# Kernel tuning notes

Measured on AMD Instinct MI355X. Metric: run time of the kernel, lower is better.

The kernel has to match this reference:

```python
import jax, jax.numpy as jnp
import numpy as np
jax.config.update("jax_enable_x64", True)

WINDOW_SHAPE = (16, 16, 8)
SPARSE_SHAPE = (512, 512, 64)
GROUP_SIZE = 128
BATCH_COUNTS = np.array([500000, 480123, 510007, 495870], dtype=np.int64)  # not multiples of 128 -> padding path active


def setup_inputs() -> dict:
    key = jax.random.key(0)
    kx, ky, kz = jax.random.split(key, 3)
    N = int(BATCH_COUNTS.sum())
    bids = jnp.asarray(np.repeat(np.arange(len(BATCH_COUNTS), dtype=np.int64), BATCH_COUNTS))
    x = jax.random.randint(kx, (N,), 0, SPARSE_SHAPE[0], dtype=jnp.int64)
    y = jax.random.randint(ky, (N,), 0, SPARSE_SHAPE[1], dtype=jnp.int64)
    z = jax.random.randint(kz, (N,), 0, SPARSE_SHAPE[2], dtype=jnp.int64)
    coords = jnp.stack([bids, x, y, z], axis=1)  # [N,4] int64: (batch, x, y, z)
    return {"coords": coords, "batch_size": 4}


def _hash_keys(coords, shifted):
    n, m, l = SPARSE_SHAPE
    n2o, m2o, l2o = WINDOW_SHAPE
    n1 = int(np.ceil(n / n2o) + 1)
    m1 = int(np.ceil(m / m2o) + 1)
    l1 = int(np.ceil(l / l2o) + 1)
    if shifted:
        x = coords[:, 1] + n2o // 2
        y = coords[:, 2] + m2o // 2
        z = coords[:, 3] + l2o // 2
    else:
        x, y, z = coords[:, 1], coords[:, 2], coords[:, 3]
    x1, y1, z1 = x // n2o, y // m2o, z // l2o
    x2, y2, z2 = x % n2o, y % m2o, z % l2o
    # original code triples both window and grid-of-window extents before hashing
    n2, m2, l2 = 3 * n2o, 3 * m2o, 3 * l2o
    n1, m1, l1 = 3 * n1, 3 * m1, 3 * l1
    sx = 1 - 2 * (x1 & 1)  # (-1)**x1
    sy = 1 - 2 * (y1 & 1)
    sz = 1 - 2 * (z1 & 1)
    s2x = 1 - 2 * (x2 & 1)
    s2y = 1 - 2 * (y2 & 1)
    s2z = 1 - 2 * (z2 & 1)
    boff = coords[:, 0] * (n * m * l * 10)
    vx = (n1 * y1 + n1 * m1 * z1 + sy * x1) * (n2 * m2 * l2) + sy * (m2 * x2 + n2 * m2 * z2 + s2x * y2) + boff
    vy = (m1 * z1 + m1 * l1 * x1 + sz * y1) * (m2 * l2 * n2) + sz * (l2 * y2 + m2 * l2 * x2 + s2y * z2) + boff
    vz = (l1 * x1 + l1 * n1 * y1 + sx * z1) * (l2 * n2 * m2) + sx * (n2 * z2 + l2 * n2 * y2 + s2z * x2) + boff
    return vx, vy, vz


def reference(coords, batch_size):
    G = GROUP_SIZE
    coords = coords.astype(jnp.int64)
    bids = coords[:, 0]
    N = coords.shape[0]
    num_per_batch = jax.ops.segment_sum(jnp.ones((N,), jnp.int64), bids, num_segments=batch_size)
    bs = jnp.concatenate([jnp.zeros((1,), jnp.int64), jnp.cumsum(num_per_batch)])
    num_per_batch_p = ((num_per_batch + G - 1) // G) * G
    bsp = jnp.concatenate([jnp.zeros((1,), jnp.int64), jnp.cumsum(num_per_batch_p)])
    Np = int(bsp[-1])  # concrete (not under jit); padded total length

    # win2flat[j] = j + (bsp[b] - bs[b]) for b = batch of element j (coords assumed batch-sorted)
    win2flat = jnp.arange(N, dtype=jnp.int64) + (bsp[:-1] - bs[:-1])[bids]

    # flat2win: identity within each padded batch, with the padded tail replicated
    # from one group earlier, then shifted back to flat indexing.
    p = jnp.arange(Np, dtype=jnp.int64)
    b = jnp.searchsorted(bsp, p, side="right") - 1  # batch of each padded slot
    r = num_per_batch % G
    pad_tail = (r[b] != 0) & (p >= bsp[b + 1] - G + r[b])
    flat2win = p - G * pad_tail.astype(jnp.int64) - (bsp[b] - bs[b])

    outs = [flat2win, win2flat]
    for shifted in (False, True):
        vx, vy, vz = _hash_keys(coords, shifted)
        outs.append(jnp.argsort(vx))
        outs.append(jnp.argsort(vy))
        outs.append(jnp.argsort(vz))
    # (flat2win, win2flat, x, y, z, x_shift, y_shift, z_shift)
    return tuple(outs)
```

## Files before the change

### kernel.cpp

```cpp
#include <hip/hip_runtime.h>
#include <type_traits>

typedef unsigned long long u64;
typedef unsigned int u32;

#define BLOCK     256
#define WAVES     4
#define TILE      4096
#define SUBT      1024
#define CHUNKS    16
#define KSHIFT    21
#define KBIAS     (1LL << 21)
#define KMASK     ((1u << 21) - 1)
#define GRP       128


__device__ __forceinline__ void hash3(long long x, long long y, long long z,
                                      long long boff, long long* v) {
  long long x1 = x >> 4, y1 = y >> 4, z1 = z >> 3;
  long long x2 = x & 15, y2 = y & 15, z2 = z & 7;
  long long sx  = 1 - 2*(x1 & 1), sy  = 1 - 2*(y1 & 1), sz  = 1 - 2*(z1 & 1);
  long long s2x = 1 - 2*(x2 & 1), s2y = 1 - 2*(y2 & 1), s2z = 1 - 2*(z2 & 1);
  v[0] = (99*y1 + 9801*z1 + sy*x1)*55296 + sy*(48*x2 + 2304*z2 + s2x*y2) + boff;
  v[1] = (99*z1 + 2673*x1 + sz*y1)*55296 + sz*(24*y2 + 1152*x2 + s2y*z2) + boff;
  v[2] = (27*x1 + 2673*y1 + sx*z1)*55296 + sx*(48*z2 + 1152*y2 + s2z*x2) + boff;
}

__global__ void count_k(const int* __restrict__ coords, unsigned* __restrict__ counts, int N) {
  __shared__ unsigned c[8];
  if (threadIdx.x < 8) c[threadIdx.x] = 0;
  __syncthreads();
  for (int i = blockIdx.x*blockDim.x + threadIdx.x; i < N; i += gridDim.x*blockDim.x)
    atomicAdd(&c[coords[4*i] & 7], 1u);
  __syncthreads();
  if (threadIdx.x < 8) atomicAdd(&counts[threadIdx.x], c[threadIdx.x]);
}

__global__ void prefix_k(const unsigned* __restrict__ counts, long long* __restrict__ meta,
                         const int* __restrict__ bsz) {
  int NB = *bsz; if (NB > 8) NB = 8;
  long long run_bs = 0, run_bsp = 0;
  meta[0] = 0;
  for (int b = 0; b < NB; b++) {
    long long c  = (long long)counts[b];
    long long cp = (c + GRP - 1) / GRP * GRP;
    long long r  = c % GRP;
    meta[9 + b]  = run_bsp - run_bs;
    meta[17 + b] = r ? (run_bsp + cp - GRP + r) : 0x7fffffffffffffffLL;
    run_bs += c; run_bsp += cp;
    meta[b + 1] = run_bsp;
  }
  meta[25] = run_bsp;
  meta[26] = NB;
}

__global__ void flat2win_k(const long long* __restrict__ meta, int* __restrict__ dout) {
  long long p = (long long)blockIdx.x * blockDim.x + threadIdx.x;
  long long Np = meta[25];
  if (p >= Np) return;
  int NB = (int)meta[26];
  int b = 0;
  while (b < NB - 1 && meta[b + 1] <= p) b++;
  long long pad = (p >= meta[17 + b]) ? 1 : 0;
  dout[p] = (int)(p - GRP * pad - meta[9 + b]);
}

__global__ void __launch_bounds__(BLOCK) keygen_k(const int* __restrict__ coords,
                                                  u64* __restrict__ keys,
                                                  u32* __restrict__ hist,
                                                  const long long* __restrict__ meta,
                                                  int* __restrict__ dout,
                                                  int N, int B, int g0, int g, int doAux) {
  __shared__ u32 cnt[6 * 256];
  int b = blockIdx.x, tid = threadIdx.x;
  int nb = g * 256;
  for (int j = tid; j < nb; j += BLOCK) cnt[j] = 0;
  __syncthreads();
  long long Np = meta[25];
  for (int t = 0; t < CHUNKS; t++) {
    int i = b * TILE + t * BLOCK + tid;
    if (i < N) {
      int4 c4 = ((const int4*)coords)[i];
      long long boff = (long long)c4.x * 167772160LL;
      long long v[6];
      hash3(c4.y,     c4.z,     c4.w,     boff, v);
      hash3(c4.y + 8, c4.z + 8, c4.w + 4, boff, v + 3);
      #pragma unroll
      for (int s = 0; s < 6; s++) {
        if (s >= g0 && s < g0 + g) {
          u64 kb = (u64)(v[s] + KBIAS);
          keys[(size_t)(s - g0) * N + i] = (kb << KSHIFT) | (unsigned)i;
          atomicAdd(&cnt[(s - g0) * 256 + ((unsigned)kb & 255)], 1u);
        }
      }
      if (doAux) dout[Np + i] = (int)(i + meta[9 + c4.x]);
    }
  }
  __syncthreads();
  for (int j = tid; j < nb; j += BLOCK) {
    int s = j >> 8, d = j & 255;
    hist[((size_t)s * B + b) * 256 + d] = cnt[j];
  }
}

template<typename KT, int RADIXN, int SHIFT>
__global__ void __launch_bounds__(BLOCK) hist_k(const KT* __restrict__ src,
                                                u32* __restrict__ hist, int N, int B) {
  __shared__ u32 cnt[RADIXN];
  int s = blockIdx.y, b = blockIdx.x, tid = threadIdx.x;
  for (int j = tid; j < RADIXN; j += BLOCK) cnt[j] = 0;
  __syncthreads();
  const KT* in = src + (size_t)s * N;
  #pragma unroll 4
  for (int t = 0; t < CHUNKS; t++) {
    int i = b * TILE + t * BLOCK + tid;
    if (i < N) {
      unsigned d = (unsigned)(in[i] >> SHIFT) & (RADIXN - 1);
      atomicAdd(&cnt[d], 1u);
    }
  }
  __syncthreads();
  for (int j = tid; j < RADIXN; j += BLOCK) hist[((size_t)s * B + b) * RADIXN + j] = cnt[j];
}

template<int RADIXN>
__global__ void __launch_bounds__(BLOCK) scan_k(u32* __restrict__ hist,
                                                u32* __restrict__ dbase, int B) {
  __shared__ u32 tot[RADIXN];
  int s = blockIdx.x, tid = threadIdx.x;
  for (int d = tid; d < RADIXN; d += BLOCK) {
    u32 run = 0; int b = 0;
    for (; b + 8 <= B; b += 8) {
      u32 v[8];
      #pragma unroll
      for (int j = 0; j < 8; j++) v[j] = hist[((size_t)s * B + b + j) * RADIXN + d];
      #pragma unroll
      for (int j = 0; j < 8; j++) { hist[((size_t)s * B + b + j) * RADIXN + d] = run; run += v[j]; }
    }
    for (; b < B; b++) {
      size_t x = ((size_t)s * B + b) * RADIXN + d;
      u32 v = hist[x]; hist[x] = run; run += v;
    }
    tot[d] = run;
  }
  __syncthreads();
  if (tid < 64) {
    u32 run = 0;
    #pragma unroll
    for (int c = 0; c < (RADIXN + 63) / 64; c++) {
      int dd = c * 64 + tid;
      u32 v = (dd < RADIXN) ? tot[dd] : 0, x = v;
      for (int off = 1; off < 64; off <<= 1) { u32 u = __shfl_up(x, off); if (tid >= off) x += u; }
      if (dd < RADIXN) dbase[(size_t)s * 512 + dd] = run + x - v;
      run += __shfl(x, 63);
    }
  }
}

template<int RB, int SHIFT, int MODE>
__global__ void __launch_bounds__(BLOCK) scatter_k(const void* __restrict__ srcv,
                                                   void* __restrict__ dstv,
                                                   const u32* __restrict__ hist,
                                                   const u32* __restrict__ dbase,
                                                   int N, int B,
                                                   int* __restrict__ dout,
                                                   const long long* __restrict__ meta, int g0) {
  constexpr int RADIXN = 1 << RB;
  constexpr int DPT = (RADIXN + BLOCK - 1) / BLOCK;
  using KT = typename std::conditional<MODE == 2, u32, u64>::type;
  using ST = typename std::conditional<MODE == 0, u64, u32>::type;
  __shared__ ST items[TILE];
  __shared__ unsigned short dig[MODE == 1 ? TILE : 64];
  __shared__ unsigned short cnt[WAVES][RADIXN];
  __shared__ int exf[RADIXN];
  int s = blockIdx.y, b = blockIdx.x, tid = threadIdx.x;
  int wave = tid >> 6, lane = tid & 63;
  for (int j = tid; j < WAVES * RADIXN; j += BLOCK) ((unsigned short*)cnt)[j] = 0;
  __syncthreads();

  const KT* in = (const KT*)srcv + (size_t)s * N;
  int subbase = b * TILE + wave * SUBT;
  bool full = (subbase + SUBT <= N);
  KT k[CHUNKS]; u32 pd[CHUNKS];
  if (full) {
    #pragma unroll
    for (int t = 0; t < CHUNKS; t++) k[t] = in[subbase + t * 64 + lane];
    #pragma unroll
    for (int t = 0; t < CHUNKS; t++) {
      unsigned d = (unsigned)(k[t] >> SHIFT) & (RADIXN - 1);
      u64 m = ~0ull;
      #pragma unroll
      for (int bit = 0; bit < RB; bit++) {
        u64 bal = __ballot((d >> bit) & 1);
        m &= ((d >> bit) & 1) ? bal : ~bal;
      }
      unsigned rank = __builtin_amdgcn_mbcnt_hi((u32)(m >> 32),
                        __builtin_amdgcn_mbcnt_lo((u32)m, 0u));
      unsigned pbase = cnt[wave][d];
      pd[t] = d | ((pbase + rank) << RB);
      if (rank == 0) cnt[wave][d] = (unsigned short)(pbase + (unsigned)__popcll(m));
    }
  } else {
    #pragma unroll
    for (int t = 0; t < CHUNKS; t++) k[t] = in[min(subbase + t * 64 + lane, N - 1)];
    #pragma unroll
    for (int t = 0; t < CHUNKS; t++) {
      int i = subbase + t * 64 + lane;
      bool valid = i < N;
      unsigned d = (unsigned)(k[t] >> SHIFT) & (RADIXN - 1);
      u64 m = __ballot(valid);
      #pragma unroll
      for (int bit = 0; bit < RB; bit++) {
        u64 bal = __ballot(valid && ((d >> bit) & 1));
        m &= ((d >> bit) & 1) ? bal : ~bal;
      }
      unsigned rank = __builtin_amdgcn_mbcnt_hi((u32)(m >> 32),
                        __builtin_amdgcn_mbcnt_lo((u32)m, 0u));
      unsigned pbase = cnt[wave][d];
      pd[t] = d | ((pbase + rank) << RB);
      if (valid && rank == 0) cnt[wave][d] = (unsigned short)(pbase + (unsigned)__popcll(m));
    }
  }
  __syncthreads();

  u32 sc[DPT][3];
  #pragma unroll
  for (int q = 0; q < DPT; q++) {
    int d = q * BLOCK + tid;
    u32 a0 = cnt[0][d], a1 = cnt[1][d], a2 = cnt[2][d], a3 = cnt[3][d];
    sc[q][0] = a0; sc[q][1] = a1; sc[q][2] = a2;
    exf[d] = (int)(a0 + a1 + a2 + a3);
  }
  __syncthreads();
  if (tid < 64) {
    u32 run = 0;
    #pragma unroll
    for (int c = 0; c < (RADIXN + 63) / 64; c++) {
      int dd = c * 64 + tid;
      u32 v = (u32)exf[dd], x = v;
      for (int off = 1; off < 64; off <<= 1) { u32 u = __shfl_up(x, off); if (tid >= off) x += u; }
      exf[dd] = (int)(run + x - v);
      run += __shfl(x, 63);
    }
  }
  __syncthreads();
  const u32* hrow = hist + (size_t)(s * B + b) * RADIXN;
  const u32* brow = dbase + (size_t)s * 512;
  #pragma unroll
  for (int q = 0; q < DPT; q++) {
    int d = q * BLOCK + tid;
    int e = exf[d];
    u32 gb = hrow[d] + brow[d];
    cnt[0][d] = (unsigned short)e;
    cnt[1][d] = (unsigned short)(e + sc[q][0]);
    cnt[2][d] = (unsigned short)(e + sc[q][0] + sc[q][1]);
    cnt[3][d] = (unsigned short)(e + sc[q][0] + sc[q][1] + sc[q][2]);
    exf[d] = (int)gb - e;
  }
  __syncthreads();

  #pragma unroll
  for (int t = 0; t < CHUNKS; t++) {
    int i = subbase + t * 64 + lane;
    if (i < N) {
      unsigned d = pd[t] & (RADIXN - 1);
      unsigned lr = pd[t] >> RB;
      unsigned pos = (unsigned)cnt[wave][d] + lr;
      if constexpr (MODE == 1) {
        items[pos] = (u32)(((k[t] >> 46) << 21) | ((u32)k[t] & KMASK));
        dig[pos] = (unsigned short)d;
      } else {
        items[pos] = (ST)k[t];
      }
    }
  }
  __syncthreads();

  int validCount = N - b * TILE; if (validCount > TILE) validCount = TILE;
  long long obase = 0;
  if (MODE == 2) obase = meta[25] + (long long)N * (1 + g0 + s);
  u64* out64 = (u64*)dstv + (size_t)s * N;
  u32* out32 = (u32*)dstv + (size_t)s * N;
  #pragma unroll 4
  for (int t = 0; t < CHUNKS; t++) {
    int j = t * BLOCK + tid;
    if (j < validCount) {
      ST kk = items[j];
      if constexpr (MODE == 0) {
        unsigned d = (unsigned)(kk >> SHIFT) & (RADIXN - 1);
        out64[exf[d] + j] = kk;
      } else if constexpr (MODE == 1) {
        unsigned d = dig[j];
        out32[exf[d] + j] = kk;
      } else {
        unsigned d = (unsigned)(kk >> SHIFT) & (RADIXN - 1);
        dout[obase + exf[d] + j] = (int)(kk & KMASK);
      }
    }
  }
}

extern "C" void kernel_launch(void* const* d_in, const int* in_sizes, int n_in,
                              void* d_out, int out_size, void* d_ws, size_t ws_size,
                              hipStream_t stream) {
  const int* coords = (const int*)d_in[0];
  const int* bsz    = (const int*)d_in[1];
  int N = in_sizes[0] / 4;
  int* dout = (int*)d_out;
  char* ws = (char*)d_ws;
  int B = (N + TILE - 1) / TILE;

  auto align256 = [](size_t x) { return (x + 255) & ~(size_t)255; };

  int g = 1;
  size_t offHist = 512, offBase = 0, offA = 0, offB = 0;
  const int cands[4] = {6, 3, 2, 1};
  for (int ci = 0; ci < 4; ci++) {
    int cg = cands[ci];
    size_t oBs = offHist + (size_t)cg * B * 512 * 4;
    size_t oA = align256(oBs + (size_t)cg * 512 * 4);
    size_t oB = oA + (size_t)cg * N * 8;
    size_t need = oB + (size_t)cg * N * 8;
    if (need <= ws_size || cg == 1) {
      g = cg; offBase = oBs; offA = oA; offB = oB;
      if (need <= ws_size) break;
    }
  }

  unsigned*  counts = (unsigned*)ws;
  long long* meta   = (long long*)(ws + 64);
  u32*       hist   = (u32*)(ws + offHist);
  u32*       dbase  = (u32*)(ws + offBase);
  u64*       keysA  = (u64*)(ws + offA);
  u64*       keysB  = (u64*)(ws + offB);

  hipMemsetAsync(ws, 0, 512, stream);
  count_k<<<1024, 256, 0, stream>>>(coords, counts, N);
  prefix_k<<<1, 1, 0, stream>>>(counts, meta, bsz);
  flat2win_k<<<(N + 8 * GRP + 255) / 256, 256, 0, stream>>>(meta, dout);

  for (int g0 = 0; g0 < 6; g0 += g) {
    keygen_k<<<B, BLOCK, 0, stream>>>(coords, keysA, hist, meta, dout, N, B, g0, g, g0 == 0);
    scan_k<256><<<g, BLOCK, 0, stream>>>(hist, dbase, B);
    scatter_k<8, 21, 0><<<dim3(B, g), BLOCK, 0, stream>>>(keysA, keysB, hist, dbase, N, B,
                                                          dout, meta, g0);
    hist_k<u64, 256, 29><<<dim3(B, g), BLOCK, 0, stream>>>(keysB, hist, N, B);
    scan_k<256><<<g, BLOCK, 0, stream>>>(hist, dbase, B);
    scatter_k<8, 29, 0><<<dim3(B, g), BLOCK, 0, stream>>>(keysB, keysA, hist, dbase, N, B,
                                                          dout, meta, g0);
    hist_k<u64, 512, 37><<<dim3(B, g), BLOCK, 0, stream>>>(keysA, hist, N, B);
    scan_k<512><<<g, BLOCK, 0, stream>>>(hist, dbase, B);
    scatter_k<9, 37, 1><<<dim3(B, g), BLOCK, 0, stream>>>(keysA, keysB, hist, dbase, N, B,
                                                          dout, meta, g0);
    hist_k<u32, 256, 21><<<dim3(B, g), BLOCK, 0, stream>>>((const u32*)keysB, hist, N, B);
    scan_k<256><<<g, BLOCK, 0, stream>>>(hist, dbase, B);
    scatter_k<8, 21, 2><<<dim3(B, g), BLOCK, 0, stream>>>(keysB, keysA, hist, dbase, N, B,
                                                          dout, meta, g0);
  }
}
```

Before: 472.5 us.

## Transpose radix histogram to digit-major layout and widen scatter blocks to 512 threads

Histograms are now stored digit-major ([slice][digit][block]), so each scan thread walks one contiguous row instead of striding by RADIXN across blocks. The scatter kernel now uses 512 threads (8 waves of 512 items each) per 4096-item tile, so each thread holds fewer keys in registers. It also loads its global base offset early, before the first barrier. The scan is launched with 512 threads so each digit gets one thread. In exchange, each lane in the scan still reads a separate row, so accesses within a wave are strided, and the per-wave counter table in scatter doubles.

```diff
diff --git a/kernel.cpp b/kernel.cpp
--- a/kernel.cpp
+++ b/kernel.cpp
@@ -5,10 +5,12 @@
 typedef unsigned int u32;
 
 #define BLOCK     256
-#define WAVES     4
 #define TILE      4096
-#define SUBT      1024
-#define CHUNKS    16
+#define HCHUNK    16
+#define SBLOCK    512
+#define SWAVES    8
+#define SSUBT     512
+#define SCH       8
 #define KSHIFT    21
 #define KBIAS     (1LL << 21)
 #define KMASK     ((1u << 21) - 1)
@@ -77,7 +79,7 @@
   for (int j = tid; j < nb; j += BLOCK) cnt[j] = 0;
   __syncthreads();
   long long Np = meta[25];
-  for (int t = 0; t < CHUNKS; t++) {
+  for (int t = 0; t < HCHUNK; t++) {
     int i = b * TILE + t * BLOCK + tid;
     if (i < N) {
       int4 c4 = ((const int4*)coords)[i];
@@ -99,7 +101,7 @@
   __syncthreads();
   for (int j = tid; j < nb; j += BLOCK) {
     int s = j >> 8, d = j & 255;
-    hist[((size_t)s * B + b) * 256 + d] = cnt[j];
+    hist[((size_t)s * 256 + d) * B + b] = cnt[j];
   }
 }
 
@@ -112,7 +114,7 @@
   __syncthreads();
   const KT* in = src + (size_t)s * N;
   #pragma unroll 4
-  for (int t = 0; t < CHUNKS; t++) {
+  for (int t = 0; t < HCHUNK; t++) {
     int i = b * TILE + t * BLOCK + tid;
     if (i < N) {
       unsigned d = (unsigned)(in[i] >> SHIFT) & (RADIXN - 1);
@@ -120,28 +122,26 @@
     }
   }
   __syncthreads();
-  for (int j = tid; j < RADIXN; j += BLOCK) hist[((size_t)s * B + b) * RADIXN + j] = cnt[j];
+  for (int j = tid; j < RADIXN; j += BLOCK) hist[((size_t)s * RADIXN + j) * B + b] = cnt[j];
 }
 
 template<int RADIXN>
-__global__ void __launch_bounds__(BLOCK) scan_k(u32* __restrict__ hist,
-                                                u32* __restrict__ dbase, int B) {
+__global__ void __launch_bounds__(512) scan_k(u32* __restrict__ hist,
+                                              u32* __restrict__ dbase, int B) {
   __shared__ u32 tot[RADIXN];
   int s = blockIdx.x, tid = threadIdx.x;
-  for (int d = tid; d < RADIXN; d += BLOCK) {
+  if (tid < RADIXN) {
+    u32* row = hist + ((size_t)s * RADIXN + tid) * B;
     u32 run = 0; int b = 0;
     for (; b + 8 <= B; b += 8) {
       u32 v[8];
       #pragma unroll
-      for (int j = 0; j < 8; j++) v[j] = hist[((size_t)s * B + b + j) * RADIXN + d];
-      #pragma unroll
-      for (int j = 0; j < 8; j++) { hist[((size_t)s * B + b + j) * RADIXN + d] = run; run += v[j]; }
-    }
-    for (; b < B; b++) {
-      size_t x = ((size_t)s * B + b) * RADIXN + d;
-      u32 v = hist[x]; hist[x] = run; run += v;
-    }
-    tot[d] = run;
+      for (int j = 0; j < 8; j++) v[j] = row[b + j];
+      #pragma unroll
+      for (int j = 0; j < 8; j++) { row[b + j] = run; run += v[j]; }
+    }
+    for (; b < B; b++) { u32 v = row[b]; row[b] = run; run += v; }
+    tot[tid] = run;
   }
   __syncthreads();
   if (tid < 64) {
@@ -158,35 +158,39 @@
 }
 
 template<int RB, int SHIFT, int MODE>
-__global__ void __launch_bounds__(BLOCK) scatter_k(const void* __restrict__ srcv,
-                                                   void* __restrict__ dstv,
-                                                   const u32* __restrict__ hist,
-                                                   const u32* __restrict__ dbase,
-                                                   int N, int B,
-                                                   int* __restrict__ dout,
-                                                   const long long* __restrict__ meta, int g0) {
+__global__ void __launch_bounds__(SBLOCK, 8) scatter_k(const void* __restrict__ srcv,
+                                                       void* __restrict__ dstv,
+                                                       const u32* __restrict__ hist,
+                                                       const u32* __restrict__ dbase,
+                                                       int N, int B,
+                                                       int* __restrict__ dout,
+                                                       const long long* __restrict__ meta, int g0) {
   constexpr int RADIXN = 1 << RB;
-  constexpr int DPT = (RADIXN + BLOCK - 1) / BLOCK;
   using KT = typename std::conditional<MODE == 2, u32, u64>::type;
   using ST = typename std::conditional<MODE == 0, u64, u32>::type;
   __shared__ ST items[TILE];
   __shared__ unsigned short dig[MODE == 1 ? TILE : 64];
-  __shared__ unsigned short cnt[WAVES][RADIXN];
+  __shared__ unsigned short cnt[SWAVES][RADIXN];
   __shared__ int exf[RADIXN];
   int s = blockIdx.y, b = blockIdx.x, tid = threadIdx.x;
   int wave = tid >> 6, lane = tid & 63;
-  for (int j = tid; j < WAVES * RADIXN; j += BLOCK) ((unsigned short*)cnt)[j] = 0;
+
+  u32 gb = 0;
+  if (tid < RADIXN)
+    gb = hist[((size_t)s * RADIXN + tid) * B + b] + dbase[(size_t)s * 512 + tid];
+
+  for (int j = tid; j < SWAVES * RADIXN; j += SBLOCK) ((unsigned short*)cnt)[j] = 0;
   __syncthreads();
 
   const KT* in = (const KT*)srcv + (size_t)s * N;
-  int subbase = b * TILE + wave * SUBT;
-  bool full = (subbase + SUBT <= N);
-  KT k[CHUNKS]; u32 pd[CHUNKS];
+  int subbase = b * TILE + wave * SSUBT;
+  bool full = (subbase + SSUBT <= N);
+  KT k[SCH]; u32 pd[SCH];
   if (full) {
     #pragma unroll
-    for (int t = 0; t < CHUNKS; t++) k[t] = in[subbase + t * 64 + lane];
-    #pragma unroll
-    for (int t = 0; t < CHUNKS; t++) {
+    for (int t = 0; t < SCH; t++) k[t] = in[subbase + t * 64 + lane];
+    #pragma unroll
+    for (int t = 0; t < SCH; t++) {
       unsigned d = (unsigned)(k[t] >> SHIFT) & (RADIXN - 1);
       u64 m = ~0ull;
       #pragma unroll
@@ -202,9 +206,9 @@
     }
   } else {
     #pragma unroll
-    for (int t = 0; t < CHUNKS; t++) k[t] = in[min(subbase + t * 64 + lane, N - 1)];
-    #pragma unroll
-    for (int t = 0; t < CHUNKS; t++) {
+    for (int t = 0; t < SCH; t++) k[t] = in[min(subbase + t * 64 + lane, N - 1)];
+    #pragma unroll
+    for (int t = 0; t < SCH; t++) {
       int i = subbase + t * 64 + lane;
       bool valid = i < N;
       unsigned d = (unsigned)(k[t] >> SHIFT) & (RADIXN - 1);
@@ -223,13 +227,12 @@
   }
   __syncthreads();
 
-  u32 sc[DPT][3];
-  #pragma unroll
-  for (int q = 0; q < DPT; q++) {
-    int d = q * BLOCK + tid;
-    u32 a0 = cnt[0][d], a1 = cnt[1][d], a2 = cnt[2][d], a3 = cnt[3][d];
-    sc[q][0] = a0; sc[q][1] = a1; sc[q][2] = a2;
-    exf[d] = (int)(a0 + a1 + a2 + a3);
+  u32 aw[SWAVES];
+  if (tid < RADIXN) {
+    u32 tt = 0;
+    #pragma unroll
+    for (int w = 0; w < SWAVES; w++) { aw[w] = cnt[w][tid]; tt += aw[w]; }
+    exf[tid] = (int)tt;
   }
   __syncthreads();
   if (tid < 64) {
@@ -237,30 +240,24 @@
     #pragma unroll
     for (int c = 0; c < (RADIXN + 63) / 64; c++) {
       int dd = c * 64 + tid;
-      u32 v = (u32)exf[dd], x = v;
+      u32 v = (dd < RADIXN) ? (u32)exf[dd] : 0, x = v;
       for (int off = 1; off < 64; off <<= 1) { u32 u = __shfl_up(x, off); if (tid >= off) x += u; }
-      exf[dd] = (int)(run + x - v);
+      if (dd < RADIXN) exf[dd] = (int)(run + x - v);
       run += __shfl(x, 63);
     }
   }
   __syncthreads();
-  const u32* hrow = hist + (size_t)(s * B + b) * RADIXN;
-  const u32* brow = dbase + (size_t)s * 512;
+  if (tid < RADIXN) {
+    int e = exf[tid];
+    u32 run = (u32)e;
+    #pragma unroll
+    for (int w = 0; w < SWAVES; w++) { cnt[w][tid] = (unsigned short)run; run += aw[w]; }
+    exf[tid] = (int)gb - e;
+  }
+  __syncthreads();
+
   #pragma unroll
-  for (int q = 0; q < DPT; q++) {
-    int d = q * BLOCK + tid;
-    int e = exf[d];
-    u32 gb = hrow[d] + brow[d];
-    cnt[0][d] = (unsigned short)e;
-    cnt[1][d] = (unsigned short)(e + sc[q][0]);
-    cnt[2][d] = (unsigned short)(e + sc[q][0] + sc[q][1]);
-    cnt[3][d] = (unsigned short)(e + sc[q][0] + sc[q][1] + sc[q][2]);
-    exf[d] = (int)gb - e;
-  }
-  __syncthreads();
-
-  #pragma unroll
-  for (int t = 0; t < CHUNKS; t++) {
+  for (int t = 0; t < SCH; t++) {
     int i = subbase + t * 64 + lane;
     if (i < N) {
       unsigned d = pd[t] & (RADIXN - 1);
@@ -281,9 +278,9 @@
   if (MODE == 2) obase = meta[25] + (long long)N * (1 + g0 + s);
   u64* out64 = (u64*)dstv + (size_t)s * N;
   u32* out32 = (u32*)dstv + (size_t)s * N;
-  #pragma unroll 4
-  for (int t = 0; t < CHUNKS; t++) {
-    int j = t * BLOCK + tid;
+  #pragma unroll
+  for (int t = 0; t < TILE / SBLOCK; t++) {
+    int j = t * SBLOCK + tid;
     if (j < validCount) {
       ST kk = items[j];
       if constexpr (MODE == 0) {
@@ -341,20 +338,20 @@
 
   for (int g0 = 0; g0 < 6; g0 += g) {
     keygen_k<<<B, BLOCK, 0, stream>>>(coords, keysA, hist, meta, dout, N, B, g0, g, g0 == 0);
-    scan_k<256><<<g, BLOCK, 0, stream>>>(hist, dbase, B);
-    scatter_k<8, 21, 0><<<dim3(B, g), BLOCK, 0, stream>>>(keysA, keysB, hist, dbase, N, B,
-                                                          dout, meta, g0);
+    scan_k<256><<<g, 512, 0, stream>>>(hist, dbase, B);
+    scatter_k<8, 21, 0><<<dim3(B, g), SBLOCK, 0, stream>>>(keysA, keysB, hist, dbase, N, B,
+                                                           dout, meta, g0);
     hist_k<u64, 256, 29><<<dim3(B, g), BLOCK, 0, stream>>>(keysB, hist, N, B);
-    scan_k<256><<<g, BLOCK, 0, stream>>>(hist, dbase, B);
-    scatter_k<8, 29, 0><<<dim3(B, g), BLOCK, 0, stream>>>(keysB, keysA, hist, dbase, N, B,
-                                                          dout, meta, g0);
+    scan_k<256><<<g, 512, 0, stream>>>(hist, dbase, B);
+    scatter_k<8, 29, 0><<<dim3(B, g), SBLOCK, 0, stream>>>(keysB, keysA, hist, dbase, N, B,
+                                                           dout, meta, g0);
     hist_k<u64, 512, 37><<<dim3(B, g), BLOCK, 0, stream>>>(keysA, hist, N, B);
-    scan_k<512><<<g, BLOCK, 0, stream>>>(hist, dbase, B);
-    scatter_k<9, 37, 1><<<dim3(B, g), BLOCK, 0, stream>>>(keysA, keysB, hist, dbase, N, B,
-                                                          dout, meta, g0);
+    scan_k<512><<<g, 512, 0, stream>>>(hist, dbase, B);
+    scatter_k<9, 37, 1><<<dim3(B, g), SBLOCK, 0, stream>>>(keysA, keysB, hist, dbase, N, B,
+                                                           dout, meta, g0);
     hist_k<u32, 256, 21><<<dim3(B, g), BLOCK, 0, stream>>>((const u32*)keysB, hist, N, B);
-    scan_k<256><<<g, BLOCK, 0, stream>>>(hist, dbase, B);
-    scatter_k<8, 21, 2><<<dim3(B, g), BLOCK, 0, stream>>>(keysB, keysA, hist, dbase, N, B,
-                                                          dout, meta, g0);
-  }
-}
+    scan_k<256><<<g, 512, 0, stream>>>(hist, dbase, B);
+    scatter_k<8, 21, 2><<<dim3(B, g), SBLOCK, 0, stream>>>(keysB, keysA, hist, dbase, N, B,
+                                                           dout, meta, g0);
+  }
+}
```

Result: slower. 711.0 us (+50.5%).
